# Kernel tuning notes

Hardware: AMD Instinct MI355X
Metric: run time of the kernel (lower is better)

## Reference

```python
import jax, jax.numpy as jnp
import numpy as np

N = 50000   # num_nodes
R = 8       # num_relations
H = 128     # hidden_l
L = 32      # num_labels
E = 1600000 # num_edges


def setup_inputs() -> dict:
    key = jax.random.key(0)
    ks = jax.random.split(key, 8)
    edge_index = jax.random.randint(ks[0], (2, E), 0, N, dtype=jnp.int64)
    edge_type = jax.random.randint(ks[1], (E,), 0, R, dtype=jnp.int64)
    # layer 1: in_channels = num_nodes (x=None -> one-hot features)
    weight1 = jax.random.normal(ks[2], (R, N, H), dtype=jnp.float32) * 0.02
    root1 = jax.random.normal(ks[3], (N, H), dtype=jnp.float32) * 0.02
    bias1 = jnp.zeros((H,), dtype=jnp.float32)
    # layer 2: hidden -> labels
    weight2 = jax.random.normal(ks[4], (R, H, L), dtype=jnp.float32) * 0.05
    root2 = jax.random.normal(ks[5], (H, L), dtype=jnp.float32) * 0.05
    bias2 = jnp.zeros((L,), dtype=jnp.float32)
    return {"weight1": weight1, "root1": root1, "bias1": bias1,
            "weight2": weight2, "root2": root2, "bias2": bias2,
            "edge_index": edge_index, "edge_type": edge_type}


def _rel_mean_agg(msg, dst, et, num_nodes, num_rel):
    """PyG RGCNConv aggr='mean': mean over incoming edges per (node, relation),
    then sum over relations. msg: [E, F]."""
    seg = dst * num_rel + et  # combined (node, relation) segment id
    sums = jax.ops.segment_sum(msg, seg, num_segments=num_nodes * num_rel)
    cnt = jax.ops.segment_sum(jnp.ones((msg.shape[0],), msg.dtype), seg,
                              num_segments=num_nodes * num_rel)
    mean = sums / jnp.maximum(cnt, 1.0)[:, None]  # zero where count==0
    return mean.reshape(num_nodes, num_rel, -1).sum(axis=1)  # [N, F]


def reference(weight1, root1, bias1, weight2, root2, bias2, edge_index, edge_type):
    src, dst = edge_index[0], edge_index[1]
    # ---- layer 1 (x=None): message = weight1[r, src] row gather ----
    msg1 = weight1[edge_type, src]                      # [E, H]
    x = _rel_mean_agg(msg1, dst, edge_type, N, R) + root1 + bias1
    x = jax.nn.relu(x)
    # ---- layer 2: per-relation matmul then gather ----
    xw = jnp.einsum('nh,rhl->nrl', x, weight2)          # [N, R, L]
    msg2 = xw[src, edge_type]                           # [E, L]
    out = _rel_mean_agg(msg2, dst, edge_type, N, R) + x @ root2 + bias2
    return jax.nn.sigmoid(out)
```

## Files before the change

### kernel.cpp

```cpp
#include <hip/hip_runtime.h>
#include <math.h>

#define NN 50000
#define RR 8
#define HH 128
#define LL 32
#define EE 1600000
#define BW 128
#define NB 391
#define PB 782

#define FMA4(A, V, C) { A.x += (V).x*(C); A.y += (V).y*(C); A.z += (V).z*(C); A.w += (V).w*(C); }

typedef __attribute__((ext_vector_type(8))) short short8_t;
typedef __attribute__((ext_vector_type(4))) float f32x4_t;

__device__ __forceinline__ float bflo(unsigned u) { return __uint_as_float(u << 16); }
__device__ __forceinline__ float bfhi(unsigned u) { return __uint_as_float(u & 0xFFFF0000u); }
__device__ __forceinline__ unsigned bfpk(float a, float b) {
    unsigned ua = __float_as_uint(a), ub = __float_as_uint(b);
    ua = (ua + 0x7FFFu + ((ua >> 16) & 1u)) >> 16;
    ub = (ub + 0x7FFFu + ((ub >> 16) & 1u)) >> 16;
    return ua | (ub << 16);
}
__device__ __forceinline__ unsigned short bf16r(float f) {
    unsigned u = __float_as_uint(f);
    return (unsigned short)((u + 0x7FFFu + ((u >> 16) & 1u)) >> 16);
}

__global__ __launch_bounds__(256) void hist_kernel(const int* __restrict__ ei,
                                                   unsigned* __restrict__ ph) {
    __shared__ unsigned h[NB];
    int blk = blockIdx.x, tid = threadIdx.x;
    for (int i = tid; i < NB; i += 256) h[i] = 0;
    __syncthreads();
    int base = blk * 2048;
#pragma unroll
    for (int k = 0; k < 8; ++k) {
        int e = base + k * 256 + tid;
        if (e < EE) atomicAdd(&h[(unsigned)ei[EE + e] >> 7], 1u);
    }
    __syncthreads();
    for (int i = tid; i < NB; i += 256) ph[blk * NB + i] = h[i];
}

__global__ __launch_bounds__(256) void bred_kernel(const unsigned* __restrict__ ph,
                                                   unsigned* __restrict__ bcnt) {
    __shared__ unsigned s[4];
    int b = blockIdx.x, t = threadIdx.x;
    unsigned v = 0;
    for (int j = t; j < PB; j += 256) v += ph[j * NB + b];
    v += __shfl_down(v, 32); v += __shfl_down(v, 16); v += __shfl_down(v, 8);
    v += __shfl_down(v, 4);  v += __shfl_down(v, 2);  v += __shfl_down(v, 1);
    if ((t & 63) == 0) s[t >> 6] = v;
    __syncthreads();
    if (t == 0) bcnt[b] = s[0] + s[1] + s[2] + s[3];
}

__global__ __launch_bounds__(512) void bscan_kernel(const unsigned* __restrict__ bcnt,
                                                    unsigned* __restrict__ boff,
                                                    unsigned* __restrict__ bcur,
                                                    unsigned* __restrict__ node_off,
                                                    unsigned* __restrict__ srcr) {
    __shared__ unsigned s[512];
    int t = threadIdx.x;
    unsigned v = (t < NB) ? bcnt[t] : 0;
    s[t] = v; __syncthreads();
    for (int off = 1; off < 512; off <<= 1) {
        unsigned u = (t >= off) ? s[t - off] : 0; __syncthreads();
        if (t >= off) s[t] += u; __syncthreads();
    }
    if (t < NB) { unsigned o = s[t] - v; boff[t] = o; bcur[t] = o; }
    if (t == 0) { boff[NB] = EE; node_off[NN] = EE; }
    if (t < 16) srcr[EE + t] = 0;
}

__global__ __launch_bounds__(256) void part_conv(const int* __restrict__ ei,
                                                 const int* __restrict__ et,
                                                 unsigned* __restrict__ bcur,
                                                 unsigned* __restrict__ tmp,
                                                 const float4* __restrict__ w1,
                                                 const float* __restrict__ w2,
                                                 uint4* __restrict__ w1b,
                                                 unsigned* __restrict__ wtb) {
    __shared__ unsigned h[NB];
    int b = blockIdx.x, tid = threadIdx.x;
    if (b >= PB) {
        if (b < PB + 25000) {
            size_t t = (size_t)(b - PB) * 256 + tid;
            float4 a = w1[2 * t], c = w1[2 * t + 1];
            uint4 o;
            o.x = bfpk(a.x, a.y); o.y = bfpk(a.z, a.w);
            o.z = bfpk(c.x, c.y); o.w = bfpk(c.z, c.w);
            w1b[t] = o;
        } else {
            int c = tid, r = c >> 5, l = c & 31;
            const float* wp = w2 + (size_t)r * HH * LL + l;
            for (int k = 0; k < HH; k += 2)
                wtb[c * 64 + (k >> 1)] = bfpk(wp[k * LL], wp[(k + 1) * LL]);
        }
        return;
    }
    for (int i = tid; i < NB; i += 256) h[i] = 0;
    __syncthreads();
    int base = b * 2048;
    unsigned pay[8]; int bk[8];
#pragma unroll
    for (int k = 0; k < 8; ++k) {
        int e = base + k * 256 + tid;
        bk[k] = -1;
        if (e < EE) {
            unsigned sN = (unsigned)ei[e], d = (unsigned)ei[EE + e], r = (unsigned)et[e];
            bk[k] = (int)(d >> 7);
            pay[k] = sN | (r << 16) | ((d & 127u) << 19);
            atomicAdd(&h[bk[k]], 1u);
        }
    }
    __syncthreads();
    for (int i = tid; i < NB; i += 256) {
        unsigned c = h[i];
        h[i] = c ? atomicAdd(&bcur[i], c) : 0u;
    }
    __syncthreads();
#pragma unroll
    for (int k = 0; k < 8; ++k)
        if (bk[k] >= 0) {
            unsigned p = atomicAdd(&h[bk[k]], 1u);
            tmp[p] = pay[k];
        }
}

__global__ __launch_bounds__(256) void finalize_kernel(const unsigned* __restrict__ boff,
                                                       const unsigned* __restrict__ tmp,
                                                       unsigned* __restrict__ node_off,
                                                       float* __restrict__ inv,
                                                       unsigned* __restrict__ srcr) {
    __shared__ unsigned cnt[BW * RR];
    __shared__ unsigned cur[BW];
    __shared__ unsigned excl[BW];
    int b = blockIdx.x, t = threadIdx.x;
    unsigned lo = boff[b], hi = boff[b + 1];
    int nn0 = b * BW;
    int nloc = NN - nn0 < BW ? NN - nn0 : BW;
    for (int i = t; i < BW * RR; i += 256) cnt[i] = 0;
    __syncthreads();
    for (unsigned i = lo + t; i < hi; i += 256) {
        unsigned v = tmp[i];
        atomicAdd(&cnt[((v >> 19) & 127u) * RR + ((v >> 16) & 7u)], 1u);
    }
    __syncthreads();
    unsigned own = 0;
    if (t < BW) {
#pragma unroll
        for (int r = 0; r < RR; ++r) own += cnt[t * RR + r];
        excl[t] = own;
    }
    __syncthreads();
    for (int off = 1; off < BW; off <<= 1) {
        unsigned u = 0;
        if (t < BW && t >= off) u = excl[t - off];
        __syncthreads();
        if (t < BW && t >= off) excl[t] += u;
        __syncthreads();
    }
    if (t < nloc) {
        unsigned o = lo + excl[t] - own;
        node_off[nn0 + t] = o;
        cur[t] = o;
    }
    __syncthreads();
    for (int i = t; i < nloc * RR; i += 256) {
        unsigned c = cnt[i];
        inv[(size_t)nn0 * RR + i] = c ? 1.f / (float)c : 0.f;
    }
    for (unsigned i = lo + t; i < hi; i += 256) {
        unsigned v = tmp[i];
        unsigned p = atomicAdd(&cur[(v >> 19) & 127u], 1u);
        srcr[p] = v & 0x7FFFFu;
    }
}

__global__ __launch_bounds__(256) void l1_gather(const unsigned* __restrict__ node_off,
                                                 const unsigned* __restrict__ srcr,
                                                 const float* __restrict__ inv,
                                                 const uint4* __restrict__ w1b,
                                                 const float* __restrict__ root1,
                                                 const float* __restrict__ bias1,
                                                 uint4* __restrict__ xb) {
    int wid = threadIdx.x >> 6, lane = threadIdx.x & 63;
    int n = blockIdx.x * 4 + wid;
    if (n >= NN) return;
    int q = lane >> 4, ql = lane & 15;
    int beg = node_off[n], end = node_off[n + 1];
    int cnt = end - beg;
    int nfull = cnt >> 4;
    float myinv = inv[n * RR + (lane & 7)];
    float4 a0 = {0.f, 0.f, 0.f, 0.f}, a1 = {0.f, 0.f, 0.f, 0.f};
    int e = beg + q;
    unsigned kp0 = srcr[e], kp1 = srcr[e + 4], kp2 = srcr[e + 8], kp3 = srcr[e + 12];
#define GATH(K, C) {                                                        \
        unsigned ss = (K) & 0xFFFFu, rr = (K) >> 16;                        \
        uint4 v = w1b[((size_t)rr * NN + ss) * 16 + ql];                    \
        a0.x = fmaf(bflo(v.x), (C), a0.x); a0.y = fmaf(bfhi(v.x), (C), a0.y); \
        a0.z = fmaf(bflo(v.y), (C), a0.z); a0.w = fmaf(bfhi(v.y), (C), a0.w); \
        a1.x = fmaf(bflo(v.z), (C), a1.x); a1.y = fmaf(bfhi(v.z), (C), a1.y); \
        a1.z = fmaf(bflo(v.w), (C), a1.z); a1.w = fmaf(bfhi(v.w), (C), a1.w); }
#pragma unroll 1
    for (int it = 0; it < nfull; ++it) {
        unsigned k0 = kp0, k1 = kp1, k2 = kp2, k3 = kp3;
        e += 16;
        kp0 = srcr[e]; kp1 = srcr[e + 4]; kp2 = srcr[e + 8]; kp3 = srcr[e + 12];
        float c0 = __shfl(myinv, (int)(k0 >> 16));
        float c1 = __shfl(myinv, (int)(k1 >> 16));
        float c2 = __shfl(myinv, (int)(k2 >> 16));
        float c3 = __shfl(myinv, (int)(k3 >> 16));
        GATH(k0, c0); GATH(k1, c1); GATH(k2, c2); GATH(k3, c3);
    }
    {
        float c0 = __shfl(myinv, (int)(kp0 >> 16));
        float c1 = __shfl(myinv, (int)(kp1 >> 16));
        float c2 = __shfl(myinv, (int)(kp2 >> 16));
        float c3 = __shfl(myinv, (int)(kp3 >> 16));
        if (e < end)      GATH(kp0, c0);
        if (e + 4 < end)  GATH(kp1, c1);
        if (e + 8 < end)  GATH(kp2, c2);
        if (e + 12 < end) GATH(kp3, c3);
    }
#undef GATH
#define RED(c) { c += __shfl_xor(c, 16); c += __shfl_xor(c, 32); }
    RED(a0.x); RED(a0.y); RED(a0.z); RED(a0.w);
    RED(a1.x); RED(a1.y); RED(a1.z); RED(a1.w);
#undef RED
    if (q == 0) {
        const float4* rt = (const float4*)(root1 + (size_t)n * HH);
        const float4* bs = (const float4*)bias1;
        float4 rA = rt[2 * ql], rB = rt[2 * ql + 1];
        float4 bA = bs[2 * ql], bB = bs[2 * ql + 1];
        float o0 = fmaxf(a0.x + rA.x + bA.x, 0.f);
        float o1 = fmaxf(a0.y + rA.y + bA.y, 0.f);
        float o2 = fmaxf(a0.z + rA.z + bA.z, 0.f);
        float o3 = fmaxf(a0.w + rA.w + bA.w, 0.f);
        float o4 = fmaxf(a1.x + rB.x + bB.x, 0.f);
        float o5 = fmaxf(a1.y + rB.y + bB.y, 0.f);
        float o6 = fmaxf(a1.z + rB.z + bB.z, 0.f);
        float o7 = fmaxf(a1.w + rB.w + bB.w, 0.f);
        uint4 o;
        o.x = bfpk(o0, o1); o.y = bfpk(o2, o3);
        o.z = bfpk(o4, o5); o.w = bfpk(o6, o7);
        xb[(size_t)n * 16 + ql] = o;
    }
}

__global__ __launch_bounds__(256) void xw_mfma(const unsigned* __restrict__ xb,
                                               const unsigned* __restrict__ wtb,
                                               unsigned short* __restrict__ xwb) {
    int tid = threadIdx.x, wid = tid >> 6, l = tid & 63;
    int bn = blockIdx.x >> 2;
    int bc = blockIdx.x & 3;
    int col = bc * 64 + wid * 16 + (l & 15);
    int kq = l >> 4;
    short8_t bfr[4];
    const unsigned* wcol = wtb + col * 64;
#pragma unroll
    for (int ks = 0; ks < 4; ++ks)
        bfr[ks] = *reinterpret_cast<const short8_t*>(wcol + ks * 16 + kq * 4);
    int n0 = bn * 64;
#pragma unroll
    for (int sub = 0; sub < 4; ++sub) {
        int row = n0 + sub * 16 + (l & 15);
        int rc = row < NN ? row : NN - 1;
        const unsigned* xr = xb + (size_t)rc * 64;
        f32x4_t acc = {0.f, 0.f, 0.f, 0.f};
#pragma unroll
        for (int ks = 0; ks < 4; ++ks) {
            short8_t a = *reinterpret_cast<const short8_t*>(xr + ks * 16 + kq * 4);
            acc = __builtin_amdgcn_mfma_f32_16x16x32_bf16(a, bfr[ks], acc, 0, 0, 0);
        }
        int orow0 = n0 + sub * 16 + kq * 4;
#pragma unroll
        for (int j = 0; j < 4; ++j) {
            int orow = orow0 + j;
            if (orow < NN) xwb[(size_t)orow * 256 + col] = bf16r(acc[j]);
        }
    }
}

__global__ __launch_bounds__(256) void l2_gather(const unsigned* __restrict__ node_off,
                                                 const unsigned* __restrict__ srcr,
                                                 const float* __restrict__ inv,
                                                 const uint2* __restrict__ xwb,
                                                 const unsigned* __restrict__ xb,
                                                 const float* __restrict__ root2,
                                                 const float* __restrict__ bias2,
                                                 float* __restrict__ out) {
    int wid = threadIdx.x >> 6, lane = threadIdx.x & 63;
    int n = blockIdx.x * 4 + wid;
    if (n >= NN) return;
    int g = lane >> 3, gl = lane & 7;
    int beg = node_off[n], end = node_off[n + 1];
    int cnt = end - beg;
    int nfull = cnt >> 4;
    float myinv = inv[n * RR + (lane & 7)];
    float4 acc = {0.f, 0.f, 0.f, 0.f};
    int e = beg + g;
    unsigned kp0 = srcr[e], kp1 = srcr[e + 8];
#define GATH2(K, C) {                                              \
        unsigned ss = (K) & 0xFFFFu, rr = (K) >> 16;               \
        uint2 v = xwb[((size_t)ss * RR + rr) * 8 + gl];            \
        acc.x = fmaf(bflo(v.x), (C), acc.x);                       \
        acc.y = fmaf(bfhi(v.x), (C), acc.y);                       \
        acc.z = fmaf(bflo(v.y), (C), acc.z);                       \
        acc.w = fmaf(bfhi(v.y), (C), acc.w); }
#pragma unroll 1
    for (int it = 0; it < nfull; ++it) {
        unsigned k0 = kp0, k1 = kp1;
        e += 16;
        kp0 = srcr[e]; kp1 = srcr[e + 8];
        float c0 = __shfl(myinv, (int)(k0 >> 16));
        float c1 = __shfl(myinv, (int)(k1 >> 16));
        GATH2(k0, c0);
        GATH2(k1, c1);
    }
    {
        float c0 = __shfl(myinv, (int)(kp0 >> 16));
        float c1 = __shfl(myinv, (int)(kp1 >> 16));
        if (e < end)     GATH2(kp0, c0);
        if (e + 8 < end) GATH2(kp1, c1);
    }
#undef GATH2
    {
        const uint4* xr = (const uint4*)(xb + (size_t)n * 64);
        uint4 u0 = xr[g * 2], u1 = xr[g * 2 + 1];
        float xv[16] = {bflo(u0.x), bfhi(u0.x), bflo(u0.y), bfhi(u0.y),
                        bflo(u0.z), bfhi(u0.z), bflo(u0.w), bfhi(u0.w),
                        bflo(u1.x), bfhi(u1.x), bflo(u1.y), bfhi(u1.y),
                        bflo(u1.z), bfhi(u1.z), bflo(u1.w), bfhi(u1.w)};
        const float4* rp = (const float4*)root2 + g * 16 * 8 + gl;
#pragma unroll
        for (int i = 0; i < 16; ++i) {
            float4 w = rp[i * 8];
            FMA4(acc, w, xv[i]);
        }
    }
#define RED3(c) { c += __shfl_xor(c, 8); c += __shfl_xor(c, 16); c += __shfl_xor(c, 32); }
    RED3(acc.x); RED3(acc.y); RED3(acc.z); RED3(acc.w);
#undef RED3
    if (lane < 8) {
        float4 b = ((const float4*)bias2)[gl];
        float4 z;
        z.x = 1.f / (1.f + expf(-(acc.x + b.x)));
        z.y = 1.f / (1.f + expf(-(acc.y + b.y)));
        z.z = 1.f / (1.f + expf(-(acc.z + b.z)));
        z.w = 1.f / (1.f + expf(-(acc.w + b.w)));
        ((float4*)(out + (size_t)n * LL))[gl] = z;
    }
}

extern "C" void kernel_launch(void* const* d_in, const int* in_sizes, int n_in,
                              void* d_out, int out_size, void* d_ws, size_t ws_size,
                              hipStream_t stream) {
    const float* w1    = (const float*)d_in[0];
    const float* root1 = (const float*)d_in[1];
    const float* bias1 = (const float*)d_in[2];
    const float* w2    = (const float*)d_in[3];
    const float* root2 = (const float*)d_in[4];
    const float* bias2 = (const float*)d_in[5];
    const int*   ei    = (const int*)d_in[6];
    const int*   et    = (const int*)d_in[7];
    float* out = (float*)d_out;

    float*    inv      = (float*)d_ws;
    unsigned* node_off = (unsigned*)(inv + 400000);
    unsigned* boff     = node_off + 50004;
    unsigned* bcur     = boff + 400;
    unsigned* bcnt     = bcur + 400;
    unsigned* ph       = bcnt + 400;
    unsigned* srcr     = ph + 305768;
    unsigned* xb       = srcr + 1600020;
    unsigned* wtb      = xb + 3200000;
    unsigned* w1b      = wtb + 16384;
    unsigned* xwb      = w1b + 25600000;
    unsigned* tmp      = xwb;

    hist_kernel<<<PB, 256, 0, stream>>>(ei, ph);
    bred_kernel<<<NB, 256, 0, stream>>>(ph, bcnt);
    bscan_kernel<<<1, 512, 0, stream>>>(bcnt, boff, bcur, node_off, srcr);
    part_conv<<<PB + 25001, 256, 0, stream>>>(ei, et, bcur, tmp,
                                              (const float4*)w1, w2, (uint4*)w1b, wtb);
    finalize_kernel<<<NB, 256, 0, stream>>>(boff, tmp, node_off, inv, srcr);
    l1_gather<<<(NN + 3) / 4, 256, 0, stream>>>(node_off, srcr, inv, (const uint4*)w1b,
                                                root1, bias1, (uint4*)xb);
    xw_mfma<<<((NN + 63) / 64) * 4, 256, 0, stream>>>(xb, wtb, (unsigned short*)xwb);
    l2_gather<<<(NN + 3) / 4, 256, 0, stream>>>(node_off, srcr, inv, (const uint2*)xwb,
                                                xb, root2, bias2, out);
}
```

Baseline: 264.3 us.

## Compute per-block bucket offsets via column scan instead of global atomics

New measurement: 275.4 us. 1.04x slower.

```diff
diff --git a/kernel.cpp b/kernel.cpp
--- a/kernel.cpp
+++ b/kernel.cpp
@@ -44,22 +44,35 @@
     for (int i = tid; i < NB; i += 256) ph[blk * NB + i] = h[i];
 }
 
-__global__ __launch_bounds__(256) void bred_kernel(const unsigned* __restrict__ ph,
+__global__ __launch_bounds__(256) void bred_kernel(unsigned* __restrict__ ph,
                                                    unsigned* __restrict__ bcnt) {
-    __shared__ unsigned s[4];
+    __shared__ unsigned s[256];
     int b = blockIdx.x, t = threadIdx.x;
-    unsigned v = 0;
-    for (int j = t; j < PB; j += 256) v += ph[j * NB + b];
-    v += __shfl_down(v, 32); v += __shfl_down(v, 16); v += __shfl_down(v, 8);
-    v += __shfl_down(v, 4);  v += __shfl_down(v, 2);  v += __shfl_down(v, 1);
-    if ((t & 63) == 0) s[t >> 6] = v;
-    __syncthreads();
-    if (t == 0) bcnt[b] = s[0] + s[1] + s[2] + s[3];
+    unsigned v[4];
+    unsigned loc = 0;
+#pragma unroll
+    for (int j = 0; j < 4; ++j) {
+        int idx = t * 4 + j;
+        v[j] = (idx < PB) ? ph[(size_t)idx * NB + b] : 0;
+        loc += v[j];
+    }
+    s[t] = loc;
+    __syncthreads();
+    for (int off = 1; off < 256; off <<= 1) {
+        unsigned u = (t >= off) ? s[t - off] : 0; __syncthreads();
+        if (t >= off) s[t] += u; __syncthreads();
+    }
+    unsigned run = (t > 0) ? s[t - 1] : 0;
+#pragma unroll
+    for (int j = 0; j < 4; ++j) {
+        int idx = t * 4 + j;
+        if (idx < PB) { unsigned c = v[j]; ph[(size_t)idx * NB + b] = run; run += c; }
+    }
+    if (t == 255) bcnt[b] = s[255];
 }
 
 __global__ __launch_bounds__(512) void bscan_kernel(const unsigned* __restrict__ bcnt,
                                                     unsigned* __restrict__ boff,
-                                                    unsigned* __restrict__ bcur,
                                                     unsigned* __restrict__ node_off,
                                                     unsigned* __restrict__ srcr) {
     __shared__ unsigned s[512];
@@ -70,14 +83,15 @@
         unsigned u = (t >= off) ? s[t - off] : 0; __syncthreads();
         if (t >= off) s[t] += u; __syncthreads();
     }
-    if (t < NB) { unsigned o = s[t] - v; boff[t] = o; bcur[t] = o; }
+    if (t < NB) boff[t] = s[t] - v;
     if (t == 0) { boff[NB] = EE; node_off[NN] = EE; }
     if (t < 16) srcr[EE + t] = 0;
 }
 
 __global__ __launch_bounds__(256) void part_conv(const int* __restrict__ ei,
                                                  const int* __restrict__ et,
-                                                 unsigned* __restrict__ bcur,
+                                                 const unsigned* __restrict__ boff,
+                                                 const unsigned* __restrict__ ph,
                                                  unsigned* __restrict__ tmp,
                                                  const float4* __restrict__ w1,
                                                  const float* __restrict__ w2,
@@ -101,33 +115,18 @@
         }
         return;
     }
-    for (int i = tid; i < NB; i += 256) h[i] = 0;
+    for (int i = tid; i < NB; i += 256) h[i] = boff[i] + ph[(size_t)b * NB + i];
     __syncthreads();
     int base = b * 2048;
-    unsigned pay[8]; int bk[8];
 #pragma unroll
     for (int k = 0; k < 8; ++k) {
         int e = base + k * 256 + tid;
-        bk[k] = -1;
         if (e < EE) {
             unsigned sN = (unsigned)ei[e], d = (unsigned)ei[EE + e], r = (unsigned)et[e];
-            bk[k] = (int)(d >> 7);
-            pay[k] = sN | (r << 16) | ((d & 127u) << 19);
-            atomicAdd(&h[bk[k]], 1u);
-        }
-    }
-    __syncthreads();
-    for (int i = tid; i < NB; i += 256) {
-        unsigned c = h[i];
-        h[i] = c ? atomicAdd(&bcur[i], c) : 0u;
-    }
-    __syncthreads();
-#pragma unroll
-    for (int k = 0; k < 8; ++k)
-        if (bk[k] >= 0) {
-            unsigned p = atomicAdd(&h[bk[k]], 1u);
-            tmp[p] = pay[k];
-        }
+            unsigned p = atomicAdd(&h[d >> 7], 1u);
+            tmp[p] = sN | (r << 16) | ((d & 127u) << 19);
+        }
+    }
 }
 
 __global__ __launch_bounds__(256) void finalize_kernel(const unsigned* __restrict__ boff,
@@ -372,8 +371,7 @@
     float*    inv      = (float*)d_ws;
     unsigned* node_off = (unsigned*)(inv + 400000);
     unsigned* boff     = node_off + 50004;
-    unsigned* bcur     = boff + 400;
-    unsigned* bcnt     = bcur + 400;
+    unsigned* bcnt     = boff + 400;
     unsigned* ph       = bcnt + 400;
     unsigned* srcr     = ph + 305768;
     unsigned* xb       = srcr + 1600020;
@@ -384,8 +382,8 @@
 
     hist_kernel<<<PB, 256, 0, stream>>>(ei, ph);
     bred_kernel<<<NB, 256, 0, stream>>>(ph, bcnt);
-    bscan_kernel<<<1, 512, 0, stream>>>(bcnt, boff, bcur, node_off, srcr);
-    part_conv<<<PB + 25001, 256, 0, stream>>>(ei, et, bcur, tmp,
+    bscan_kernel<<<1, 512, 0, stream>>>(bcnt, boff, node_off, srcr);
+    part_conv<<<PB + 25001, 256, 0, stream>>>(ei, et, boff, ph, tmp,
                                               (const float4*)w1, w2, (uint4*)w1b, wtb);
     finalize_kernel<<<NB, 256, 0, stream>>>(boff, tmp, node_off, inv, srcr);
     l1_gather<<<(NN + 3) / 4, 256, 0, stream>>>(node_off, srcr, inv, (const uint4*)w1b,
```
